# Kernel tuning notes

Hardware: AMD Instinct MI355X
Metric: run time of the kernel (lower is better)

Reference implementation:

```python
import jax, jax.numpy as jnp
import numpy as np

CLIP_MIN = 0.0  # recurrent_clip_min resolved in build() when -1
CLIP_MAX = 1.0  # recurrent_clip_max default when timesteps unknown


def setup_inputs() -> dict:
    key = jax.random.key(0)
    k1, k2, k3 = jax.random.split(key, 3)
    B, T, D, U = 64, 512, 256, 512
    x = jax.random.normal(k1, (B, T, D), dtype=jnp.float32)
    h0 = jnp.zeros((B, U), dtype=jnp.float32)
    W = jax.random.normal(k2, (D, U), dtype=jnp.float32) * (1.0 / np.sqrt(D))
    u = jax.random.uniform(k3, (U,), dtype=jnp.float32)  # uniform in clip range
    b = jnp.zeros((U,), dtype=jnp.float32)
    return {"x": x, "h0": h0, "W": W, "u": u, "b": b}


def reference(x, h0, W, u, b):
    # IndRNN: h_t = relu(x_t @ W + h_{t-1} * u + b), u clipped to [0, 1]
    u_c = jnp.clip(u, CLIP_MIN, CLIP_MAX)
    # One-time input projection for all timesteps: [B,T,U]
    proj = jnp.einsum("btd,du->btu", x, W) + b
    proj_t = jnp.swapaxes(proj, 0, 1)  # [T,B,U] for scan over time

    def step(h, p_t):
        h_new = jax.nn.relu(p_t + h * u_c)
        return h_new, h_new

    _, hs = jax.lax.scan(step, h0, proj_t)  # hs: [T,B,U]
    return jnp.swapaxes(hs, 0, 1)  # [B,T,U]
```

## Files before the change

### kernel.cpp

```cpp
#include <hip/hip_runtime.h>


__device__ __forceinline__ unsigned short f2bf(float f) {
    unsigned int u = __float_as_uint(f);
    unsigned int r = (u + 0x7FFF + ((u >> 16) & 1)) >> 16;
    return (unsigned short)r;
}

typedef __bf16 bf16x8 __attribute__((ext_vector_type(8)));
typedef float f32x4 __attribute__((ext_vector_type(4)));

typedef const unsigned char __attribute__((address_space(1))) gc_t;
typedef unsigned char __attribute__((address_space(3))) lds_t;

__device__ __forceinline__ void gl_lds16(const void* g, void* l) {
    __builtin_amdgcn_global_load_lds((gc_t*)g, (lds_t*)l, 16, 0, 0);
}

__global__ __launch_bounds__(256) void conv_x(
    const float* __restrict__ x, unsigned short* __restrict__ xb, int n4)
{
    int i = blockIdx.x * blockDim.x + threadIdx.x;
    if (i >= n4) return;
    float4 v = *(const float4*)(x + (long)i * 4);
    ushort4 o;
    o.x = f2bf(v.x); o.y = f2bf(v.y); o.z = f2bf(v.z); o.w = f2bf(v.w);
    *(ushort4*)(xb + (long)i * 4) = o;
}

__global__ __launch_bounds__(256) void conv_wt(
    const float* __restrict__ W, unsigned short* __restrict__ Wt, int K, int N)
{
    int idx = blockIdx.x * blockDim.x + threadIdx.x;
    int kq = K >> 2;
    if (idx >= N * kq) return;
    int n = idx / kq;
    int k4 = (idx - n * kq) * 4;
    ushort4 o;
    o.x = f2bf(W[(long)(k4 + 0) * N + n]);
    o.y = f2bf(W[(long)(k4 + 1) * N + n]);
    o.z = f2bf(W[(long)(k4 + 2) * N + n]);
    o.w = f2bf(W[(long)(k4 + 3) * N + n]);
    *(ushort4*)(Wt + (long)n * K + k4) = o;
}

#define GBM 128
#define GBN 128
#define GBK 32

__global__ __launch_bounds__(256) void gemm_mfma(
    const unsigned short* __restrict__ Ab,
    const unsigned short* __restrict__ Btb,
    const float* __restrict__ bias,
    float* __restrict__ C, int M, int N, int K)
{
    __shared__ __bf16 As[GBM * GBK];
    __shared__ __bf16 Bs[GBN * GBK];

    const int tid  = threadIdx.x;
    const int lane = tid & 63;
    const int w    = tid >> 6;
    const int m    = lane & 15;
    const int quad = lane >> 4;
    const int row0 = blockIdx.x * GBM;
    const int col0 = blockIdx.y * GBN;

    const int sr = lane >> 2;
    const int sg = ((lane & 3) - ((sr >> 1) & 3)) & 3;
    const int slot = (((m >> 1) & 3) + quad) & 3;

    f32x4 acc[4][4];
#pragma unroll
    for (int i = 0; i < 4; ++i)
#pragma unroll
        for (int j = 0; j < 4; ++j) acc[i][j] = (f32x4){0.f, 0.f, 0.f, 0.f};

    const int rowA_base = (w >> 1) * 64;
    const int colB_base = (w & 1) * 64;

    for (int kt = 0; kt < K; kt += GBK) {
#pragma unroll
        for (int c = 0; c < 2; ++c) {
            int rt = w * 32 + c * 16;
            const unsigned short* ga =
                Ab + (long)(row0 + rt + sr) * K + kt + sg * 8;
            gl_lds16(ga, (void*)(As + (rt)*GBK));
            const unsigned short* gb =
                Btb + (long)(col0 + rt + sr) * K + kt + sg * 8;
            gl_lds16(gb, (void*)(Bs + (rt)*GBK));
        }
        __syncthreads();

        bf16x8 af[4], bf[4];
#pragma unroll
        for (int i = 0; i < 4; ++i) {
            int rowA = rowA_base + i * 16 + m;
            af[i] = *(const bf16x8*)(As + rowA * GBK + slot * 8);
            int rowB = colB_base + i * 16 + m;
            bf[i] = *(const bf16x8*)(Bs + rowB * GBK + slot * 8);
        }
#pragma unroll
        for (int i = 0; i < 4; ++i)
#pragma unroll
            for (int j = 0; j < 4; ++j)
                acc[i][j] = __builtin_amdgcn_mfma_f32_16x16x32_bf16(
                    af[i], bf[j], acc[i][j], 0, 0, 0);
        __syncthreads();
    }

    float bb[4];
#pragma unroll
    for (int j = 0; j < 4; ++j) bb[j] = bias[col0 + colB_base + j * 16 + m];

#pragma unroll
    for (int i = 0; i < 4; ++i) {
#pragma unroll
        for (int r = 0; r < 4; ++r) {
            int row = row0 + rowA_base + i * 16 + quad * 4 + r;
            float* crow = C + (long)row * N + col0 + colB_base + m;
#pragma unroll
            for (int j = 0; j < 4; ++j)
                crow[j * 16] = acc[i][j][r] + bb[j];
        }
    }
}

#define BM 128
#define BN 128
#define BK 8

__global__ __launch_bounds__(256) void indrnn_gemm_bias(
    const float* __restrict__ A, const float* __restrict__ Bm,
    const float* __restrict__ bias, float* __restrict__ C,
    int M, int N, int K)
{
    __shared__ float As[BK][BM];
    __shared__ float Bs[BK][BN];
    const int tid = threadIdx.x;
    const int row0 = blockIdx.x * BM, col0 = blockIdx.y * BN;
    const int tx = tid & 15, ty = tid >> 4;
    float acc[8][8];
#pragma unroll
    for (int i = 0; i < 8; ++i)
#pragma unroll
        for (int j = 0; j < 8; ++j) acc[i][j] = 0.0f;
    const int am = tid >> 1, ak = (tid & 1) * 4;
    const int bk = tid >> 5, bn = (tid & 31) * 4;
    const float* Aptr = A + (long)(row0 + am) * K + ak;
    const float* Bptr = Bm + (long)bk * N + col0 + bn;
    for (int kt = 0; kt < K; kt += BK) {
        float4 av = *(const float4*)(Aptr + kt);
        float4 bv = *(const float4*)(Bptr + (long)kt * N);
        As[ak + 0][am] = av.x; As[ak + 1][am] = av.y;
        As[ak + 2][am] = av.z; As[ak + 3][am] = av.w;
        *(float4*)&Bs[bk][bn] = bv;
        __syncthreads();
#pragma unroll
        for (int k = 0; k < BK; ++k) {
            float4 a0 = *(const float4*)&As[k][ty * 4];
            float4 a1 = *(const float4*)&As[k][64 + ty * 4];
            float4 b0 = *(const float4*)&Bs[k][tx * 4];
            float4 b1 = *(const float4*)&Bs[k][64 + tx * 4];
            float a[8] = {a0.x, a0.y, a0.z, a0.w, a1.x, a1.y, a1.z, a1.w};
            float b[8] = {b0.x, b0.y, b0.z, b0.w, b1.x, b1.y, b1.z, b1.w};
#pragma unroll
            for (int i = 0; i < 8; ++i)
#pragma unroll
                for (int j = 0; j < 8; ++j)
                    acc[i][j] = fmaf(a[i], b[j], acc[i][j]);
        }
        __syncthreads();
    }
    float bb[8];
#pragma unroll
    for (int j = 0; j < 4; ++j) {
        bb[j] = bias[col0 + tx * 4 + j];
        bb[j + 4] = bias[col0 + 64 + tx * 4 + j];
    }
#pragma unroll
    for (int i = 0; i < 8; ++i) {
        const int r = (i < 4) ? (ty * 4 + i) : (64 + ty * 4 + (i - 4));
        float* crow = C + (long)(row0 + r) * N + col0;
        float4 v0 = {acc[i][0] + bb[0], acc[i][1] + bb[1], acc[i][2] + bb[2], acc[i][3] + bb[3]};
        float4 v1 = {acc[i][4] + bb[4], acc[i][5] + bb[5], acc[i][6] + bb[6], acc[i][7] + bb[7]};
        *(float4*)(crow + tx * 4) = v0;
        *(float4*)(crow + 64 + tx * 4) = v1;
    }
}

#define SCAN_UNROLL 32

__global__ __launch_bounds__(256) void indrnn_scan(
    float* __restrict__ out, const float* __restrict__ h0,
    const float* __restrict__ u, int B, int T, int U)
{
    const int idx = blockIdx.x * blockDim.x + threadIdx.x;
    if (idx >= B * U) return;
    const int b = idx / U;
    const int un = idx - b * U;

    const float uc = fminf(fmaxf(u[un], 0.0f), 1.0f);
    float h = h0[(long)b * U + un];
    float* p = out + (long)b * T * U + un;

    for (int t = 0; t < T; t += SCAN_UNROLL) {
        float pv[SCAN_UNROLL];
#pragma unroll
        for (int i = 0; i < SCAN_UNROLL; ++i)
            pv[i] = p[(long)(t + i) * U];
#pragma unroll
        for (int i = 0; i < SCAN_UNROLL; ++i) {
            h = fmaxf(fmaf(h, uc, pv[i]), 0.0f);
            pv[i] = h;
        }
#pragma unroll
        for (int i = 0; i < SCAN_UNROLL; ++i)
            p[(long)(t + i) * U] = pv[i];
    }
}

extern "C" void kernel_launch(void* const* d_in, const int* in_sizes, int n_in,
                              void* d_out, int out_size, void* d_ws, size_t ws_size,
                              hipStream_t stream) {
    const float* x  = (const float*)d_in[0];
    const float* h0 = (const float*)d_in[1];
    const float* W  = (const float*)d_in[2];
    const float* u  = (const float*)d_in[3];
    const float* b  = (const float*)d_in[4];
    float* out = (float*)d_out;

    const int U = in_sizes[3];
    const int B = in_sizes[1] / U;
    const int D = in_sizes[2] / U;
    const int T = in_sizes[0] / (B * D);
    const int M = B * T;

    const size_t xb_bytes = (size_t)M * D * sizeof(unsigned short);
    const size_t wt_bytes = (size_t)U * D * sizeof(unsigned short);
    const bool use_mfma = (ws_size >= xb_bytes + wt_bytes) &&
                          (M % GBM == 0) && (U % GBN == 0) && (D % GBK == 0);

    if (use_mfma) {
        unsigned short* xb = (unsigned short*)d_ws;
        unsigned short* wt = (unsigned short*)((char*)d_ws + xb_bytes);

        const int n4 = (M * D) / 4;
        conv_x<<<(n4 + 255) / 256, 256, 0, stream>>>(x, xb, n4);

        const int nwt = U * (D / 4);
        conv_wt<<<(nwt + 255) / 256, 256, 0, stream>>>(W, wt, D, U);

        dim3 ggrid(M / GBM, U / GBN);
        gemm_mfma<<<ggrid, 256, 0, stream>>>(xb, wt, b, out, M, U, D);
    } else {
        dim3 ggrid(M / BM, U / BN);
        indrnn_gemm_bias<<<ggrid, 256, 0, stream>>>(x, W, b, out, M, U, D);
    }

    const int nthreads = B * U;
    indrnn_scan<<<(nthreads + 255) / 256, 256, 0, stream>>>(out, h0, u, B, T, U);
}
```

Baseline: 138.4 us.

## Fuse bf16 MFMA projection with IndRNN scan per batch and column tile

Replaces the separate MFMA GEMM and scan kernels with one fused kernel. Each block owns one batch row and a 128-column slice, holds its W slice in registers, and streams x in 64-timestep chunks through double-buffered LDS. The projection lands in swizzled LDS, where half the threads run the recurrence and write the output while the other half prefetch the next chunk. This removes the write and re-read of the full projection through global memory, but the grid is only 256 blocks at one block per CU, and the scan is serialised per chunk.

```diff
diff --git a/kernel.cpp b/kernel.cpp
--- a/kernel.cpp
+++ b/kernel.cpp
@@ -44,83 +44,123 @@
     *(ushort4*)(Wt + (long)n * K + k4) = o;
 }
 
-#define GBM 128
-#define GBN 128
-#define GBK 32
-
-__global__ __launch_bounds__(256) void gemm_mfma(
-    const unsigned short* __restrict__ Ab,
-    const unsigned short* __restrict__ Btb,
+#define TC 64
+#define GN 128
+
+__global__ __launch_bounds__(256, 1) void indrnn_fused(
+    const unsigned short* __restrict__ xb,
+    const unsigned short* __restrict__ wt,
     const float* __restrict__ bias,
-    float* __restrict__ C, int M, int N, int K)
-{
-    __shared__ __bf16 As[GBM * GBK];
-    __shared__ __bf16 Bs[GBN * GBK];
+    const float* __restrict__ h0,
+    const float* __restrict__ uvec,
+    float* __restrict__ out,
+    int B, int T, int U)
+{
+    __shared__ char X[2][TC * 512];
 
     const int tid  = threadIdx.x;
     const int lane = tid & 63;
     const int w    = tid >> 6;
     const int m    = lane & 15;
     const int quad = lane >> 4;
-    const int row0 = blockIdx.x * GBM;
-    const int col0 = blockIdx.y * GBN;
-
-    const int sr = lane >> 2;
-    const int sg = ((lane & 3) - ((sr >> 1) & 3)) & 3;
-    const int slot = (((m >> 1) & 3) + quad) & 3;
-
-    f32x4 acc[4][4];
-#pragma unroll
-    for (int i = 0; i < 4; ++i)
-#pragma unroll
-        for (int j = 0; j < 4; ++j) acc[i][j] = (f32x4){0.f, 0.f, 0.f, 0.f};
-
-    const int rowA_base = (w >> 1) * 64;
-    const int colB_base = (w & 1) * 64;
-
-    for (int kt = 0; kt < K; kt += GBK) {
-#pragma unroll
-        for (int c = 0; c < 2; ++c) {
-            int rt = w * 32 + c * 16;
-            const unsigned short* ga =
-                Ab + (long)(row0 + rt + sr) * K + kt + sg * 8;
-            gl_lds16(ga, (void*)(As + (rt)*GBK));
-            const unsigned short* gb =
-                Btb + (long)(col0 + rt + sr) * K + kt + sg * 8;
-            gl_lds16(gb, (void*)(Bs + (rt)*GBK));
-        }
-        __syncthreads();
-
-        bf16x8 af[4], bf[4];
-#pragma unroll
-        for (int i = 0; i < 4; ++i) {
-            int rowA = rowA_base + i * 16 + m;
-            af[i] = *(const bf16x8*)(As + rowA * GBK + slot * 8);
-            int rowB = colB_base + i * 16 + m;
-            bf[i] = *(const bf16x8*)(Bs + rowB * GBK + slot * 8);
-        }
-#pragma unroll
-        for (int i = 0; i < 4; ++i)
+    const int b    = blockIdx.x;
+    const int n0   = blockIdx.y * GN;
+    const int tq   = (w >> 1) * 32;
+    const int cq   = (w & 1) * 64;
+
+    bf16x8 bfr[4][8];
+#pragma unroll
+    for (int j = 0; j < 4; ++j)
+#pragma unroll
+        for (int kt = 0; kt < 8; ++kt)
+            bfr[j][kt] = *(const bf16x8*)(
+                wt + (long)(n0 + cq + j * 16 + m) * 256 + kt * 32 + quad * 8);
+
+    float bb[4];
+#pragma unroll
+    for (int j = 0; j < 4; ++j) bb[j] = bias[n0 + cq + j * 16 + m];
+
+    float uc = 0.0f, h = 0.0f;
+    if (tid < GN) {
+        uc = fminf(fmaxf(uvec[n0 + tid], 0.0f), 1.0f);
+        h  = h0[(long)b * U + n0 + tid];
+    }
+
+    const unsigned short* xrow = xb + (long)b * T * 256;
+
+    {
+        const int p = lane & 31, hh = lane >> 5;
+#pragma unroll
+        for (int i = 0; i < 8; ++i) {
+            int blk = i * 4 + w;
+            int row = blk * 2 + hh;
+            int gp  = p ^ (row & 15);
+            gl_lds16(xrow + (long)row * 256 + gp * 8, &X[0][blk * 1024]);
+        }
+    }
+
+    const int nch = T / TC;
+    for (int c = 0; c < nch; ++c) {
+        char* Xc = X[c & 1];
+        __syncthreads();
+
+        f32x4 acc[2][4];
+#pragma unroll
+        for (int i = 0; i < 2; ++i)
+#pragma unroll
+            for (int j = 0; j < 4; ++j) acc[i][j] = (f32x4){0.f, 0.f, 0.f, 0.f};
+
+#pragma unroll
+        for (int kt = 0; kt < 8; ++kt) {
+            const int off = (((kt * 4 + quad) ^ m) * 16);
+            bf16x8 a0 = *(const bf16x8*)(Xc + (tq + m) * 512 + off);
+            bf16x8 a1 = *(const bf16x8*)(Xc + (tq + 16 + m) * 512 + off);
+#pragma unroll
+            for (int j = 0; j < 4; ++j) {
+                acc[0][j] = __builtin_amdgcn_mfma_f32_16x16x32_bf16(
+                    a0, bfr[j][kt], acc[0][j], 0, 0, 0);
+                acc[1][j] = __builtin_amdgcn_mfma_f32_16x16x32_bf16(
+                    a1, bfr[j][kt], acc[1][j], 0, 0, 0);
+            }
+        }
+        __syncthreads();
+
+        float* pf = (float*)Xc;
+#pragma unroll
+        for (int i = 0; i < 2; ++i)
 #pragma unroll
             for (int j = 0; j < 4; ++j)
-                acc[i][j] = __builtin_amdgcn_mfma_f32_16x16x32_bf16(
-                    af[i], bf[j], acc[i][j], 0, 0, 0);
-        __syncthreads();
-    }
-
-    float bb[4];
-#pragma unroll
-    for (int j = 0; j < 4; ++j) bb[j] = bias[col0 + colB_base + j * 16 + m];
-
-#pragma unroll
-    for (int i = 0; i < 4; ++i) {
-#pragma unroll
-        for (int r = 0; r < 4; ++r) {
-            int row = row0 + rowA_base + i * 16 + quad * 4 + r;
-            float* crow = C + (long)row * N + col0 + colB_base + m;
-#pragma unroll
-            for (int j = 0; j < 4; ++j)
-                crow[j * 16] = acc[i][j][r] + bb[j];
+#pragma unroll
+                for (int r = 0; r < 4; ++r) {
+                    int tl  = tq + i * 16 + quad * 4 + r;
+                    int col = cq + j * 16 + m;
+                    int cs  = col ^ (quad << 4);
+                    pf[tl * GN + cs] = acc[i][j][r] + bb[j];
+                }
+        __syncthreads();
+
+        if (tid >= 128) {
+            if (c + 1 < nch) {
+                char* Xn = X[(c + 1) & 1];
+                const unsigned short* gb = xrow + (long)(c + 1) * TC * 256;
+                const int p = lane & 31, hh = lane >> 5;
+#pragma unroll
+                for (int i = 0; i < 16; ++i) {
+                    int blk = i * 2 + (w - 2);
+                    int row = blk * 2 + hh;
+                    int gp  = p ^ (row & 15);
+                    gl_lds16(gb + (long)row * 256 + gp * 8, Xn + blk * 1024);
+                }
+            }
+        } else {
+            const float* pfr = (const float*)Xc;
+            float* og = out + ((long)b * T + c * TC) * U + n0 + tid;
+#pragma unroll 8
+            for (int t = 0; t < TC; ++t) {
+                float pv = pfr[t * GN + (tid ^ (((t >> 2) & 3) << 4))];
+                h = fmaxf(fmaf(h, uc, pv), 0.0f);
+                og[(long)t * U] = h;
+            }
         }
     }
 }
@@ -162,12 +202,12 @@
             float4 b0 = *(const float4*)&Bs[k][tx * 4];
             float4 b1 = *(const float4*)&Bs[k][64 + tx * 4];
             float a[8] = {a0.x, a0.y, a0.z, a0.w, a1.x, a1.y, a1.z, a1.w};
-            float b[8] = {b0.x, b0.y, b0.z, b0.w, b1.x, b1.y, b1.z, b1.w};
+            float bb2[8] = {b0.x, b0.y, b0.z, b0.w, b1.x, b1.y, b1.z, b1.w};
 #pragma unroll
             for (int i = 0; i < 8; ++i)
 #pragma unroll
                 for (int j = 0; j < 8; ++j)
-                    acc[i][j] = fmaf(a[i], b[j], acc[i][j]);
+                    acc[i][j] = fmaf(a[i], bb2[j], acc[i][j]);
         }
         __syncthreads();
     }
@@ -198,11 +238,9 @@
     if (idx >= B * U) return;
     const int b = idx / U;
     const int un = idx - b * U;
-
     const float uc = fminf(fmaxf(u[un], 0.0f), 1.0f);
     float h = h0[(long)b * U + un];
     float* p = out + (long)b * T * U + un;
-
     for (int t = 0; t < T; t += SCAN_UNROLL) {
         float pv[SCAN_UNROLL];
 #pragma unroll
@@ -237,26 +275,24 @@
 
     const size_t xb_bytes = (size_t)M * D * sizeof(unsigned short);
     const size_t wt_bytes = (size_t)U * D * sizeof(unsigned short);
-    const bool use_mfma = (ws_size >= xb_bytes + wt_bytes) &&
-                          (M % GBM == 0) && (U % GBN == 0) && (D % GBK == 0);
-
-    if (use_mfma) {
+    const bool fused_ok = (D == 256) && (U % GN == 0) && (T % TC == 0) &&
+                          (ws_size >= xb_bytes + wt_bytes);
+
+    if (fused_ok) {
         unsigned short* xb = (unsigned short*)d_ws;
         unsigned short* wt = (unsigned short*)((char*)d_ws + xb_bytes);
 
         const int n4 = (M * D) / 4;
         conv_x<<<(n4 + 255) / 256, 256, 0, stream>>>(x, xb, n4);
-
         const int nwt = U * (D / 4);
         conv_wt<<<(nwt + 255) / 256, 256, 0, stream>>>(W, wt, D, U);
 
-        dim3 ggrid(M / GBM, U / GBN);
-        gemm_mfma<<<ggrid, 256, 0, stream>>>(xb, wt, b, out, M, U, D);
+        dim3 g(B, U / GN);
+        indrnn_fused<<<g, 256, 0, stream>>>(xb, wt, b, h0, u, out, B, T, U);
     } else {
         dim3 ggrid(M / BM, U / BN);
         indrnn_gemm_bias<<<ggrid, 256, 0, stream>>>(x, W, b, out, M, U, D);
-    }
-
-    const int nthreads = B * U;
-    indrnn_scan<<<(nthreads + 255) / 256, 256, 0, stream>>>(out, h0, u, B, T, U);
-}
+        const int nthreads = B * U;
+        indrnn_scan<<<(nthreads + 255) / 256, 256, 0, stream>>>(out, h0, u, B, T, U);
+    }
+}
```

After: 121.1 us. -12.5%, faster.

## Fuse x bf16 conversion into GEMM and store projection as bf16 for scan

Applied to the files above, without the earlier changes.

Drops the separate x-to-bf16 conversion kernel: the GEMM now loads fp32 x tiles straight into LDS through swizzled global_load_lds and packs them to bf16 in registers before the MFMA. The projection is written to workspace as bf16 rather than fp32 into the output, and a new scan kernel with 64-thread blocks reads the bf16 projection and writes the fp32 output. This removes one kernel launch and a full round trip of the bf16 x buffer, and halves projection traffic. The costs are extra LDS footprint for the fp32 A tile, packing work inside the inner loop, and bf16 rounding of the projection before the scan.

```diff
diff --git a/kernel.cpp b/kernel.cpp
--- a/kernel.cpp
+++ b/kernel.cpp
@@ -17,15 +17,10 @@
     __builtin_amdgcn_global_load_lds((gc_t*)g, (lds_t*)l, 16, 0, 0);
 }
 
-__global__ __launch_bounds__(256) void conv_x(
-    const float* __restrict__ x, unsigned short* __restrict__ xb, int n4)
-{
-    int i = blockIdx.x * blockDim.x + threadIdx.x;
-    if (i >= n4) return;
-    float4 v = *(const float4*)(x + (long)i * 4);
-    ushort4 o;
-    o.x = f2bf(v.x); o.y = f2bf(v.y); o.z = f2bf(v.z); o.w = f2bf(v.w);
-    *(ushort4*)(xb + (long)i * 4) = o;
+union bfu { bf16x8 v; unsigned u32[4]; };
+
+__device__ __forceinline__ unsigned pk2(float lo, float hi) {
+    return (unsigned)f2bf(lo) | ((unsigned)f2bf(hi) << 16);
 }
 
 __global__ __launch_bounds__(256) void conv_wt(
@@ -44,30 +39,40 @@
     *(ushort4*)(Wt + (long)n * K + k4) = o;
 }
 
-#define GBM 128
-#define GBN 128
-#define GBK 32
-
-__global__ __launch_bounds__(256) void gemm_mfma(
-    const unsigned short* __restrict__ Ab,
-    const unsigned short* __restrict__ Btb,
+#define QM 128
+#define QN 128
+#define QK 32
+
+__global__ __launch_bounds__(256) void gemm_proj(
+    const float* __restrict__ x,
+    const unsigned short* __restrict__ Wt,
     const float* __restrict__ bias,
-    float* __restrict__ C, int M, int N, int K)
-{
-    __shared__ __bf16 As[GBM * GBK];
-    __shared__ __bf16 Bs[GBN * GBK];
+    unsigned short* __restrict__ proj,
+    int M, int N, int K)
+{
+    __shared__ __align__(16) float  As[QM * QK];
+    __shared__ __align__(16) __bf16 Bs[QN * QK];
 
     const int tid  = threadIdx.x;
     const int lane = tid & 63;
     const int w    = tid >> 6;
     const int m    = lane & 15;
     const int quad = lane >> 4;
-    const int row0 = blockIdx.x * GBM;
-    const int col0 = blockIdx.y * GBN;
-
+    const int col0 = blockIdx.x * QN;
+    const int row0 = blockIdx.y * QM;
+
+    const int rowA_base = (w >> 1) * 64;
+    const int colB_base = (w & 1) * 64;
+
+    const int ar = lane >> 3;
+    const int ap = lane & 7;
     const int sr = lane >> 2;
     const int sg = ((lane & 3) - ((sr >> 1) & 3)) & 3;
-    const int slot = (((m >> 1) & 3) + quad) & 3;
+    const int bslot = (((m >> 1) & 3) + quad) & 3;
+
+    const int af_ = ((m & 3) << 1) ^ ((m >> 2) & 1);
+    const int ag0 = (2 * quad) ^ af_;
+    const int ag1 = (2 * quad + 1) ^ af_;
 
     f32x4 acc[4][4];
 #pragma unroll
@@ -75,36 +80,43 @@
 #pragma unroll
         for (int j = 0; j < 4; ++j) acc[i][j] = (f32x4){0.f, 0.f, 0.f, 0.f};
 
-    const int rowA_base = (w >> 1) * 64;
-    const int colB_base = (w & 1) * 64;
-
-    for (int kt = 0; kt < K; kt += GBK) {
+    for (int kt = 0; kt < K; kt += QK) {
+#pragma unroll
+        for (int c = 0; c < 4; ++c) {
+            int rb = w * 32 + c * 8;
+            int r  = rb + ar;
+            int gp = ap ^ ((r & 3) << 1) ^ ((r >> 2) & 1);
+            gl_lds16(x + (long)(row0 + r) * 256 + kt + gp * 4,
+                     (char*)As + rb * 128);
+        }
 #pragma unroll
         for (int c = 0; c < 2; ++c) {
             int rt = w * 32 + c * 16;
-            const unsigned short* ga =
-                Ab + (long)(row0 + rt + sr) * K + kt + sg * 8;
-            gl_lds16(ga, (void*)(As + (rt)*GBK));
-            const unsigned short* gb =
-                Btb + (long)(col0 + rt + sr) * K + kt + sg * 8;
-            gl_lds16(gb, (void*)(Bs + (rt)*GBK));
+            gl_lds16(Wt + (long)(col0 + rt + sr) * 256 + kt + sg * 8,
+                     (char*)Bs + rt * 64);
         }
         __syncthreads();
 
-        bf16x8 af[4], bf[4];
+        bfu af[4];
+        bf16x8 bf[4];
 #pragma unroll
         for (int i = 0; i < 4; ++i) {
-            int rowA = rowA_base + i * 16 + m;
-            af[i] = *(const bf16x8*)(As + rowA * GBK + slot * 8);
-            int rowB = colB_base + i * 16 + m;
-            bf[i] = *(const bf16x8*)(Bs + rowB * GBK + slot * 8);
+            const float* ab = As + (rowA_base + i * 16 + m) * 32;
+            f32x4 p0 = *(const f32x4*)(ab + ag0 * 4);
+            f32x4 p1 = *(const f32x4*)(ab + ag1 * 4);
+            af[i].u32[0] = pk2(p0.x, p0.y);
+            af[i].u32[1] = pk2(p0.z, p0.w);
+            af[i].u32[2] = pk2(p1.x, p1.y);
+            af[i].u32[3] = pk2(p1.z, p1.w);
+            bf[i] = *(const bf16x8*)(Bs + (colB_base + i * 16 + m) * 32 +
+                                     bslot * 8);
         }
 #pragma unroll
         for (int i = 0; i < 4; ++i)
 #pragma unroll
             for (int j = 0; j < 4; ++j)
                 acc[i][j] = __builtin_amdgcn_mfma_f32_16x16x32_bf16(
-                    af[i], bf[j], acc[i][j], 0, 0, 0);
+                    af[i].v, bf[j], acc[i][j], 0, 0, 0);
         __syncthreads();
     }
 
@@ -113,15 +125,49 @@
     for (int j = 0; j < 4; ++j) bb[j] = bias[col0 + colB_base + j * 16 + m];
 
 #pragma unroll
-    for (int i = 0; i < 4; ++i) {
+    for (int i = 0; i < 4; ++i)
 #pragma unroll
         for (int r = 0; r < 4; ++r) {
             int row = row0 + rowA_base + i * 16 + quad * 4 + r;
-            float* crow = C + (long)row * N + col0 + colB_base + m;
+            unsigned short* prow =
+                proj + (long)row * N + col0 + colB_base + m;
 #pragma unroll
             for (int j = 0; j < 4; ++j)
-                crow[j * 16] = acc[i][j][r] + bb[j];
-        }
+                prow[j * 16] = f2bf(acc[i][j][r] + bb[j]);
+        }
+}
+
+#define SU 32
+
+__global__ __launch_bounds__(64) void scan_bf(
+    const unsigned short* __restrict__ proj,
+    const float* __restrict__ h0, const float* __restrict__ u,
+    float* __restrict__ out, int B, int T, int U)
+{
+    const int idx = blockIdx.x * 64 + threadIdx.x;
+    const int b = idx / U;
+    const int un = idx - b * U;
+
+    const float uc = fminf(fmaxf(u[un], 0.0f), 1.0f);
+    float h = h0[(long)b * U + un];
+    const unsigned short* p = proj + (long)b * T * U + un;
+    float* o = out + (long)b * T * U + un;
+
+    for (int t = 0; t < T; t += SU) {
+        float pv[SU];
+#pragma unroll
+        for (int i = 0; i < SU; ++i) {
+            unsigned bits = (unsigned)p[(long)(t + i) * U] << 16;
+            pv[i] = __uint_as_float(bits);
+        }
+#pragma unroll
+        for (int i = 0; i < SU; ++i) {
+            h = fmaxf(fmaf(h, uc, pv[i]), 0.0f);
+            pv[i] = h;
+        }
+#pragma unroll
+        for (int i = 0; i < SU; ++i)
+            o[(long)(t + i) * U] = pv[i];
     }
 }
 
@@ -162,12 +208,12 @@
             float4 b0 = *(const float4*)&Bs[k][tx * 4];
             float4 b1 = *(const float4*)&Bs[k][64 + tx * 4];
             float a[8] = {a0.x, a0.y, a0.z, a0.w, a1.x, a1.y, a1.z, a1.w};
-            float b[8] = {b0.x, b0.y, b0.z, b0.w, b1.x, b1.y, b1.z, b1.w};
+            float bb2[8] = {b0.x, b0.y, b0.z, b0.w, b1.x, b1.y, b1.z, b1.w};
 #pragma unroll
             for (int i = 0; i < 8; ++i)
 #pragma unroll
                 for (int j = 0; j < 8; ++j)
-                    acc[i][j] = fmaf(a[i], b[j], acc[i][j]);
+                    acc[i][j] = fmaf(a[i], bb2[j], acc[i][j]);
         }
         __syncthreads();
     }
@@ -188,8 +234,6 @@
     }
 }
 
-#define SCAN_UNROLL 32
-
 __global__ __launch_bounds__(256) void indrnn_scan(
     float* __restrict__ out, const float* __restrict__ h0,
     const float* __restrict__ u, int B, int T, int U)
@@ -198,23 +242,21 @@
     if (idx >= B * U) return;
     const int b = idx / U;
     const int un = idx - b * U;
-
     const float uc = fminf(fmaxf(u[un], 0.0f), 1.0f);
     float h = h0[(long)b * U + un];
     float* p = out + (long)b * T * U + un;
-
-    for (int t = 0; t < T; t += SCAN_UNROLL) {
-        float pv[SCAN_UNROLL];
-#pragma unroll
-        for (int i = 0; i < SCAN_UNROLL; ++i)
+    for (int t = 0; t < T; t += SU) {
+        float pv[SU];
+#pragma unroll
+        for (int i = 0; i < SU; ++i)
             pv[i] = p[(long)(t + i) * U];
 #pragma unroll
-        for (int i = 0; i < SCAN_UNROLL; ++i) {
+        for (int i = 0; i < SU; ++i) {
             h = fmaxf(fmaf(h, uc, pv[i]), 0.0f);
             pv[i] = h;
         }
 #pragma unroll
-        for (int i = 0; i < SCAN_UNROLL; ++i)
+        for (int i = 0; i < SU; ++i)
             p[(long)(t + i) * U] = pv[i];
     }
 }
@@ -235,28 +277,27 @@
     const int T = in_sizes[0] / (B * D);
     const int M = B * T;
 
-    const size_t xb_bytes = (size_t)M * D * sizeof(unsigned short);
-    const size_t wt_bytes = (size_t)U * D * sizeof(unsigned short);
-    const bool use_mfma = (ws_size >= xb_bytes + wt_bytes) &&
-                          (M % GBM == 0) && (U % GBN == 0) && (D % GBK == 0);
-
-    if (use_mfma) {
-        unsigned short* xb = (unsigned short*)d_ws;
-        unsigned short* wt = (unsigned short*)((char*)d_ws + xb_bytes);
-
-        const int n4 = (M * D) / 4;
-        conv_x<<<(n4 + 255) / 256, 256, 0, stream>>>(x, xb, n4);
+    const size_t proj_bytes = (size_t)M * U * sizeof(unsigned short);
+    const size_t wt_bytes   = (size_t)U * D * sizeof(unsigned short);
+    const bool ok = (D == 256) && (M % QM == 0) && (U % QN == 0) &&
+                    (T % SU == 0) && ((B * U) % 64 == 0) &&
+                    (ws_size >= proj_bytes + wt_bytes);
+
+    if (ok) {
+        unsigned short* proj = (unsigned short*)d_ws;
+        unsigned short* wt   = (unsigned short*)((char*)d_ws + proj_bytes);
 
         const int nwt = U * (D / 4);
         conv_wt<<<(nwt + 255) / 256, 256, 0, stream>>>(W, wt, D, U);
 
-        dim3 ggrid(M / GBM, U / GBN);
-        gemm_mfma<<<ggrid, 256, 0, stream>>>(xb, wt, b, out, M, U, D);
+        dim3 gg(U / QN, M / QM);
+        gemm_proj<<<gg, 256, 0, stream>>>(x, wt, b, proj, M, U, D);
+
+        scan_bf<<<(B * U) / 64, 64, 0, stream>>>(proj, h0, u, out, B, T, U);
     } else {
         dim3 ggrid(M / BM, U / BN);
         indrnn_gemm_bias<<<ggrid, 256, 0, stream>>>(x, W, b, out, M, U, D);
-    }
-
-    const int nthreads = B * U;
-    indrnn_scan<<<(nthreads + 255) / 256, 256, 0, stream>>>(out, h0, u, B, T, U);
-}
+        const int nthreads = B * U;
+        indrnn_scan<<<(nthreads + 255) / 256, 256, 0, stream>>>(out, h0, u, B, T, U);
+    }
+}
```

Result: faster. 134.2 us (-3.0%).
